# Optimization experiments

Measured on AMD Instinct MI355X. Metric: run time of the kernel, lower is better.

The kernel has to match this reference:

```python
import jax, jax.numpy as jnp
import numpy as np

B, N, DIM = 16, 1024, 768
H = 12
HD = DIM // H
SCALE = HD ** -0.5

def setup_inputs() -> dict:
    key = jax.random.key(0)
    k1, k2, k3, k4 = jax.random.split(key, 4)
    x = jax.random.normal(k1, (B, N, DIM), dtype=jnp.float32)
    # qkv: Linear(dim, 3*dim, bias=False); torch weight is [out, in]
    w_qkv = jax.random.normal(k2, (3 * DIM, DIM), dtype=jnp.float32) * (DIM ** -0.5)
    # proj: Linear(dim, dim) with bias
    w_proj = jax.random.normal(k3, (DIM, DIM), dtype=jnp.float32) * (DIM ** -0.5)
    b_proj = jax.random.normal(k4, (DIM,), dtype=jnp.float32) * 0.02
    return {"x": x, "w_qkv": w_qkv, "w_proj": w_proj, "b_proj": b_proj}

def reference(x, w_qkv, w_proj, b_proj):
    B_, N_, D_ = x.shape
    # qkv projection: [B, N, 3*D] -> [3, B, H, N, HD]
    qkv = jnp.einsum('bnd,ed->bne', x, w_qkv)
    qkv = qkv.reshape(B_, N_, 3, H, HD).transpose(2, 0, 3, 1, 4)
    q, k, v = qkv[0], qkv[1], qkv[2]
    # attention scores [B, H, N, N]
    attn = jnp.einsum('bhqd,bhkd->bhqk', q, k) * SCALE
    attn = jax.nn.softmax(attn, axis=-1)
    # weighted values -> [B, N, D]
    out = jnp.einsum('bhqk,bhkd->bhqd', attn, v)
    out = out.transpose(0, 2, 1, 3).reshape(B_, N_, D_)
    # output projection
    out = jnp.einsum('bnd,ed->bne', out, w_proj) + b_proj
    return out
```

## Files before the change

### kernel.cpp

```cpp
#include <hip/hip_runtime.h>
#include <cstdint>

#define B_SZ 16
#define SEQ 1024
#define DIM 768
#define NH 12
#define HD 64
#define M_TOTAL (B_SZ*SEQ)
#define QKV_OUT (3*DIM)
#define EXP2_SCALE 0.18033688011f

typedef _Float16 f16;
typedef __attribute__((ext_vector_type(8))) f16 f16x8;
typedef __attribute__((ext_vector_type(4))) f16 f16x4;
typedef __attribute__((ext_vector_type(2))) __fp16 pk16x2;
typedef __attribute__((ext_vector_type(4))) short s4_t;
typedef __attribute__((ext_vector_type(4))) float f32x4;
typedef unsigned int u32;
typedef const __attribute__((address_space(1))) u32* gas_t;
typedef __attribute__((address_space(3))) u32* las_t;

union U4 { pk16x2 h2[2]; f16x4 v; };
union U8 { pk16x2 h2[4]; f16x8 v; };
union HS { f16 h; short s; };

__device__ __forceinline__ void async16(const void* g, void* l) {
    __builtin_amdgcn_global_load_lds((gas_t)g, (las_t)l, 16, 0, 0);
}
__device__ __forceinline__ f32x4 mfma32h(f16x8 a, f16x8 b, f32x4 c) {
    return __builtin_amdgcn_mfma_f32_16x16x32_f16(a, b, c, 0, 0, 0);
}
__device__ __forceinline__ f16x8 ldfragh(const short* p) {
    return *(const f16x8*)p;
}

__global__ void cvt_kernel(const float* __restrict__ x, const float* __restrict__ wq,
                           const float* __restrict__ wp,
                           short* __restrict__ xb, short* __restrict__ wqb, short* __restrict__ wpb) {
    const long nx = (long)M_TOTAL * DIM / 4;
    const long nq = (long)QKV_OUT * DIM / 4;
    const long np = (long)DIM * DIM / 4;
    const long total = nx + nq + np;
    for (long i = (long)blockIdx.x * blockDim.x + threadIdx.x; i < total;
         i += (long)gridDim.x * blockDim.x) {
        const float4* src; short* dst; long off;
        if (i < nx)            { src = (const float4*)x;  dst = xb;  off = i; }
        else if (i < nx + nq)  { src = (const float4*)wq; dst = wqb; off = i - nx; }
        else                   { src = (const float4*)wp; dst = wpb; off = i - nx - nq; }
        float4 v = src[off];
        U4 u;
        u.h2[0] = __builtin_amdgcn_cvt_pkrtz(v.x, v.y);
        u.h2[1] = __builtin_amdgcn_cvt_pkrtz(v.z, v.w);
        *(f16x4*)(dst + off * 4) = u.v;
    }
}

template<int MH, int NHH>
__device__ __forceinline__ void mfma_quad(f32x4 (&acc)[4][6], const f16x8 (&af)[2][2],
                                          const f16x8 (&bf)[3][2]) {
#pragma unroll
    for (int r = 0; r < 2; ++r)
#pragma unroll
        for (int c = 0; c < 3; ++c) {
            f32x4 t = acc[MH * 2 + r][NHH * 3 + c];
            t = mfma32h(af[r][0], bf[c][0], t);
            t = mfma32h(af[r][1], bf[c][1], t);
            acc[MH * 2 + r][NHH * 3 + c] = t;
        }
}

template<int EPI, int N, int K>
__global__ __launch_bounds__(512, 2) void gemm_bt(const short* __restrict__ A,
                                                  const short* __restrict__ Bm,
                                                  short* __restrict__ Cq, short* __restrict__ Ck,
                                                  short* __restrict__ Cv,
                                                  float* __restrict__ Cout,
                                                  const float* __restrict__ bias) {
    static_assert(K % 128 == 0, "even K-tile count required");
    constexpr int NT = K / 64;
    constexpr int NIT = NT / 2;
    constexpr int SLOT = 28672;
    __shared__ short lds[2 * SLOT];

    const int tid = threadIdx.x;
    const int l = tid & 63, quad = l >> 4, l15 = l & 15, l7 = l15 & 7;
    const int w = tid >> 6, wr = w >> 1, wc = w & 1;

    const int gx = gridDim.x;
    const int nwg = gx * (int)gridDim.y;
    int fid = (int)blockIdx.y * gx + (int)blockIdx.x;
    fid = (fid & 7) * (nwg >> 3) + (fid >> 3);
    const int m0 = (fid / gx) * 256;
    const int n0 = (fid % gx) * 192;

    const int srow = tid >> 3, sc = tid & 7;
    const int scc = sc ^ (srow & 7);
    const short* Asrc = A + (size_t)(m0 + srow) * K + scc * 8;
    const short* Bsrc = Bm + (size_t)(n0 + srow) * K + scc * 8;
    const int sdst = tid * 8;

#define STAGE_A(t, u) async16(Asrc + (size_t)((u) * 64) * K + (t) * 64, \
                              &lds[((t) & 1) * SLOT + (u) * 4096 + sdst])
#define STAGE_B(t, u) async16(Bsrc + (size_t)((u) * 64) * K + (t) * 64, \
                              &lds[((t) & 1) * SLOT + 16384 + (u) * 4096 + sdst])

    const int awoff = wr * 4096 + l15 * 64;
    const int bwoff = 16384 + wc * 6144 + l15 * 64;
    const int c0 = (quad ^ l7) * 8;
    const int c1 = ((4 + quad) ^ l7) * 8;

#define RD_A(SB, MH) do {                                      \
        const int ab_ = (SB) + awoff + (MH) * 2048;            \
        af[0][0] = ldfragh(&lds[ab_ + c0]);                    \
        af[0][1] = ldfragh(&lds[ab_ + c1]);                    \
        af[1][0] = ldfragh(&lds[ab_ + 1024 + c0]);             \
        af[1][1] = ldfragh(&lds[ab_ + 1024 + c1]);             \
    } while (0)
#define RD_B(SB, NHH) do {                                     \
        const int bb_ = (SB) + bwoff + (NHH) * 3072;           \
        bf[0][0] = ldfragh(&lds[bb_ + c0]);                    \
        bf[0][1] = ldfragh(&lds[bb_ + c1]);                    \
        bf[1][0] = ldfragh(&lds[bb_ + 1024 + c0]);             \
        bf[1][1] = ldfragh(&lds[bb_ + 1024 + c1]);             \
        bf[2][0] = ldfragh(&lds[bb_ + 2048 + c0]);             \
        bf[2][1] = ldfragh(&lds[bb_ + 2048 + c1]);             \
    } while (0)

#define BAR1() __builtin_amdgcn_s_barrier()
#define BAR2() do { __builtin_amdgcn_s_barrier(); __builtin_amdgcn_sched_barrier(0); } while (0)
#define VMC3() asm volatile("s_waitcnt vmcnt(3)" ::: "memory")
#define VMC0() asm volatile("s_waitcnt vmcnt(0)" ::: "memory")
#define MQ(MH, NHH) do {                                       \
        __builtin_amdgcn_s_setprio(1);                         \
        mfma_quad<MH, NHH>(acc, af, bf);                       \
        __builtin_amdgcn_s_setprio(0);                         \
    } while (0)

    f32x4 acc[4][6];
#pragma unroll
    for (int i = 0; i < 4; ++i)
#pragma unroll
        for (int j = 0; j < 6; ++j) acc[i][j] = (f32x4){0.f, 0.f, 0.f, 0.f};
    f16x8 af[2][2], bf[3][2];

    STAGE_B(0, 0); STAGE_B(0, 1); STAGE_B(0, 2);
    STAGE_A(0, 0); STAGE_A(0, 1); STAGE_A(0, 2); STAGE_A(0, 3);
    STAGE_B(1, 0); STAGE_B(1, 1); STAGE_B(1, 2);
    VMC3();
    BAR2();

#pragma unroll 1
    for (int i = 0; i < NIT; ++i) {
        const int ta = 2 * i, tb = 2 * i + 1;
        {
            const int t1 = ta + 1, t2 = ta + 2;
            RD_A(0, 0); RD_B(0, 0);
            if (t1 < NT) { STAGE_A(t1, 0); STAGE_A(t1, 1); }
            BAR1(); MQ(0, 0); BAR2();

            RD_A(0, 1);
            if (t1 < NT) { STAGE_A(t1, 2); STAGE_A(t1, 3); }
            BAR1(); MQ(1, 0); BAR2();

            RD_B(0, 1);
            BAR1(); MQ(1, 1); BAR2();

            RD_A(0, 0);
            if (t2 < NT) { STAGE_B(t2, 0); STAGE_B(t2, 1); STAGE_B(t2, 2); }
            BAR1(); MQ(0, 1);
            if (t2 < NT) VMC3(); else VMC0();
            BAR2();
        }
        {
            const int t1 = tb + 1, t2 = tb + 2;
            RD_A(SLOT, 0); RD_B(SLOT, 0);
            if (t1 < NT) { STAGE_A(t1, 0); STAGE_A(t1, 1); }
            BAR1(); MQ(0, 0); BAR2();

            RD_A(SLOT, 1);
            if (t1 < NT) { STAGE_A(t1, 2); STAGE_A(t1, 3); }
            BAR1(); MQ(1, 0); BAR2();

            RD_B(SLOT, 1);
            BAR1(); MQ(1, 1); BAR2();

            RD_A(SLOT, 0);
            if (t2 < NT) { STAGE_B(t2, 0); STAGE_B(t2, 1); STAGE_B(t2, 2); }
            BAR1(); MQ(0, 1);
            if (t2 < NT) VMC3(); else VMC0();
            BAR2();
        }
    }
#undef STAGE_A
#undef STAGE_B
#undef RD_A
#undef RD_B

#pragma unroll
    for (int rt = 0; rt < 4; ++rt) {
        const int mrow = m0 + wr * 64 + (rt >> 1) * 32 + (rt & 1) * 16 + quad * 4;
#pragma unroll
        for (int ct = 0; ct < 6; ++ct) {
            const int col = n0 + wc * 96 + (ct / 3) * 48 + (ct % 3) * 16 + l15;
            if (EPI == 0) {
                int s = col / DIM;
                int h = (col - s * DIM) >> 6, hd = col & 63;
                int b = mrow >> 10, nn = mrow & 1023;
                if (s == 2) {
                    U4 u;
                    u.h2[0] = __builtin_amdgcn_cvt_pkrtz(acc[rt][ct][0], acc[rt][ct][1]);
                    u.h2[1] = __builtin_amdgcn_cvt_pkrtz(acc[rt][ct][2], acc[rt][ct][3]);
                    *(f16x4*)&Cv[(((size_t)b * NH + h) * HD + hd) * SEQ + nn] = u.v;
                } else {
                    short* dst = (s == 0) ? Cq : Ck;
                    const float qs = (s == 0) ? EXP2_SCALE : 1.0f;
#pragma unroll
                    for (int r = 0; r < 4; ++r) {
                        HS t; t.h = (f16)(acc[rt][ct][r] * qs);
                        dst[(((size_t)b * NH + h) * SEQ + nn + r) * HD + hd] = t.s;
                    }
                }
            } else {
                float bv = bias[col];
#pragma unroll
                for (int r = 0; r < 4; ++r)
                    Cout[(size_t)(mrow + r) * N + col] = acc[rt][ct][r] + bv;
            }
        }
    }
}

__global__ __launch_bounds__(256) void attn_kernel(const short* __restrict__ Q,
                                                   const short* __restrict__ Km,
                                                   const short* __restrict__ Vt,
                                                   short* __restrict__ O) {
    __shared__ short lds[3][8192];
    const int tid = threadIdx.x;
    const int w = tid >> 6, l = tid & 63, quad = l >> 4, l15 = l & 15;
    const int bid = blockIdx.x;
    const int xcd = bid & 7, kk = bid >> 3;
    const int head = xcd + 8 * (kk >> 2);
    const int q0 = (kk & 3) * 256 + w * 64;
    const int b = head / NH, h = head - b * NH;
    const short* Qp = Q + (size_t)head * (SEQ * HD);
    const short* Kp = Km + (size_t)head * (SEQ * HD);
    const short* Vp = Vt + (size_t)head * (SEQ * HD);

    f16x8 qf[4][2];
#pragma unroll
    for (int qt = 0; qt < 4; ++qt)
#pragma unroll
        for (int hf = 0; hf < 2; ++hf)
            qf[qt][hf] = *(const f16x8*)&Qp[(q0 + qt * 16 + l15) * HD + hf * 32 + quad * 8];

    f32x4 oacc[4][4];
#pragma unroll
    for (int qt = 0; qt < 4; ++qt)
#pragma unroll
        for (int ht = 0; ht < 4; ++ht) oacc[qt][ht] = (f32x4){0.f, 0.f, 0.f, 0.f};
    float psum[4] = {0.f, 0.f, 0.f, 0.f};

    const int kr = tid >> 3, kc = tid & 7;
    const int kcc = kc ^ ((kr & 3) ^ (((kr >> 3) & 3) << 1));
    const short* kSrc = Kp + kr * HD + kcc * 8;
    const int kDst = kr * 64 + kc * 8;
    const int vr = tid >> 2, vc = tid & 3;
    const int vcc = vc ^ ((vr >> 1) & 3);
    const short* vSrc = Vp + vr * SEQ + vcc * 8;
    const int vDst = 4096 + vr * 32 + vc * 8;

#define STAGE(bf, g) do {                                            \
        async16(kSrc + (size_t)(g) * 64 * HD, &lds[bf][kDst]);       \
        async16(kSrc + (size_t)((g) * 64 + 32) * HD,                 \
                &lds[bf][kDst + 2048]);                              \
        async16(vSrc + (g) * 64, &lds[bf][vDst]);                    \
        async16(vSrc + (g) * 64 + 32, &lds[bf][vDst + 2048]);        \
    } while (0)

    const int rA = 8 * (l15 >> 2) + (l15 & 3);
    const int sk = (l15 & 3) ^ ((l15 >> 2) << 1);
    const int offK = rA * 64 + ((quad ^ sk) * 8);
    const int offV = 4096 + l15 * 32 + ((quad ^ ((l15 >> 1) & 3)) * 8);

    STAGE(0, 0); STAGE(1, 1);

    int cur = 0, nb = 2;
    for (int g = 0; g < 16; ++g) {
        if (g <= 14) asm volatile("s_waitcnt vmcnt(4)" ::: "memory");
        else         asm volatile("s_waitcnt vmcnt(0)" ::: "memory");
        __builtin_amdgcn_s_barrier();
        if (g < 14) STAGE(nb, g + 2);

        const short* bufp = &lds[cur][0];
#pragma unroll
        for (int half = 0; half < 2; ++half) {
            const short* kb = bufp + half * 2048;
            f16x8 kA0 = ldfragh(kb + offK);
            f16x8 kA1 = ldfragh(kb + (offK ^ 32));
            f16x8 kB0 = ldfragh(kb + offK + 256);
            f16x8 kB1 = ldfragh(kb + (offK ^ 32) + 256);
            f16x8 v0 = ldfragh(kb + offV);
            f16x8 v1 = ldfragh(kb + offV + 512);
            f16x8 v2 = ldfragh(kb + offV + 1024);
            f16x8 v3 = ldfragh(kb + offV + 1536);

            __builtin_amdgcn_s_setprio(1);
#pragma unroll
            for (int qt = 0; qt < 4; ++qt) {
                f32x4 sA = (f32x4){0.f, 0.f, 0.f, 0.f};
                sA = mfma32h(kA0, qf[qt][0], sA);
                sA = mfma32h(kA1, qf[qt][1], sA);
                f32x4 sB = (f32x4){0.f, 0.f, 0.f, 0.f};
                sB = mfma32h(kB0, qf[qt][0], sB);
                sB = mfma32h(kB1, qf[qt][1], sB);
                float eA0 = __builtin_amdgcn_exp2f(sA[0]);
                float eA1 = __builtin_amdgcn_exp2f(sA[1]);
                float eA2 = __builtin_amdgcn_exp2f(sA[2]);
                float eA3 = __builtin_amdgcn_exp2f(sA[3]);
                float eB0 = __builtin_amdgcn_exp2f(sB[0]);
                float eB1 = __builtin_amdgcn_exp2f(sB[1]);
                float eB2 = __builtin_amdgcn_exp2f(sB[2]);
                float eB3 = __builtin_amdgcn_exp2f(sB[3]);
                psum[qt] += ((eA0 + eA1) + (eA2 + eA3)) + ((eB0 + eB1) + (eB2 + eB3));
                U8 u;
                u.h2[0] = __builtin_amdgcn_cvt_pkrtz(eA0, eA1);
                u.h2[1] = __builtin_amdgcn_cvt_pkrtz(eA2, eA3);
                u.h2[2] = __builtin_amdgcn_cvt_pkrtz(eB0, eB1);
                u.h2[3] = __builtin_amdgcn_cvt_pkrtz(eB2, eB3);
                oacc[qt][0] = mfma32h(v0, u.v, oacc[qt][0]);
                oacc[qt][1] = mfma32h(v1, u.v, oacc[qt][1]);
                oacc[qt][2] = mfma32h(v2, u.v, oacc[qt][2]);
                oacc[qt][3] = mfma32h(v3, u.v, oacc[qt][3]);
            }
            __builtin_amdgcn_s_setprio(0);
        }
        cur = (cur == 2) ? 0 : cur + 1;
        nb = (nb == 2) ? 0 : nb + 1;
    }
#undef STAGE

#pragma unroll
    for (int qt = 0; qt < 4; ++qt) {
        psum[qt] += __shfl_xor(psum[qt], 16);
        psum[qt] += __shfl_xor(psum[qt], 32);
    }

#pragma unroll
    for (int qt = 0; qt < 4; ++qt) {
        float rinv = 1.0f / psum[qt];
        short* orow = &O[((size_t)b * SEQ + q0 + qt * 16 + l15) * DIM + h * HD + quad * 4];
#pragma unroll
        for (int ht = 0; ht < 4; ++ht) {
            U4 u;
            u.h2[0] = __builtin_amdgcn_cvt_pkrtz(oacc[qt][ht][0] * rinv, oacc[qt][ht][1] * rinv);
            u.h2[1] = __builtin_amdgcn_cvt_pkrtz(oacc[qt][ht][2] * rinv, oacc[qt][ht][3] * rinv);
            *(f16x4*)(orow + ht * 16) = u.v;
        }
    }
}

extern "C" void kernel_launch(void* const* d_in, const int* in_sizes, int n_in,
                              void* d_out, int out_size, void* d_ws, size_t ws_size,
                              hipStream_t stream) {
    const float* x      = (const float*)d_in[0];
    const float* w_qkv  = (const float*)d_in[1];
    const float* w_proj = (const float*)d_in[2];
    const float* b_proj = (const float*)d_in[3];
    float* out = (float*)d_out;

    short* p = (short*)d_ws;
    short* Xb  = p; p += (size_t)M_TOTAL * DIM;
    short* Wqb = p; p += (size_t)QKV_OUT * DIM;
    short* Wpb = p; p += (size_t)DIM * DIM;
    short* Qb  = p; p += (size_t)B_SZ * NH * SEQ * HD;
    short* Kb  = p; p += (size_t)B_SZ * NH * SEQ * HD;
    short* Vtb = p; p += (size_t)B_SZ * NH * SEQ * HD;
    short* Ob  = p; p += (size_t)M_TOTAL * DIM;

    cvt_kernel<<<1024, 256, 0, stream>>>(x, w_qkv, w_proj, Xb, Wqb, Wpb);
    gemm_bt<0, QKV_OUT, DIM><<<dim3(QKV_OUT / 192, M_TOTAL / 256), 512, 0, stream>>>(
        Xb, Wqb, Qb, Kb, Vtb, nullptr, nullptr);
    attn_kernel<<<B_SZ * NH * (SEQ / 256), 256, 0, stream>>>(Qb, Kb, Vtb, Ob);
    gemm_bt<1, DIM, DIM><<<dim3(DIM / 192, M_TOTAL / 256), 512, 0, stream>>>(
        Ob, Wpb, nullptr, nullptr, nullptr, out, b_proj);
}
```

Baseline: 275.3 us.

## Restructure GEMM k-loop to load all fragments then issue all MFMAs per tile

Replaces the four-phase interleaved schedule, which alternated LDS fragment reads, partial MFMA quads and staggered async stages, with a simpler per-tile body. Each tile now waits on vmcnt, loads all A and B fragments from LDS at once, runs the full 4x6 MFMA block, and then issues the async loads for tile t+2. The epilogue row and column mapping changes to match the flat fragment indexing. This removes barriers and phase bookkeeping but needs more fragment registers and cuts the overlap of LDS reads with MFMA work and of global loads with compute.

```diff
diff --git a/kernel.cpp b/kernel.cpp
--- a/kernel.cpp
+++ b/kernel.cpp
@@ -55,20 +55,6 @@
     }
 }
 
-template<int MH, int NHH>
-__device__ __forceinline__ void mfma_quad(f32x4 (&acc)[4][6], const f16x8 (&af)[2][2],
-                                          const f16x8 (&bf)[3][2]) {
-#pragma unroll
-    for (int r = 0; r < 2; ++r)
-#pragma unroll
-        for (int c = 0; c < 3; ++c) {
-            f32x4 t = acc[MH * 2 + r][NHH * 3 + c];
-            t = mfma32h(af[r][0], bf[c][0], t);
-            t = mfma32h(af[r][1], bf[c][1], t);
-            acc[MH * 2 + r][NHH * 3 + c] = t;
-        }
-}
-
 template<int EPI, int N, int K>
 __global__ __launch_bounds__(512, 2) void gemm_bt(const short* __restrict__ A,
                                                   const short* __restrict__ Bm,
@@ -109,31 +95,50 @@
     const int c0 = (quad ^ l7) * 8;
     const int c1 = ((4 + quad) ^ l7) * 8;
 
-#define RD_A(SB, MH) do {                                      \
-        const int ab_ = (SB) + awoff + (MH) * 2048;            \
-        af[0][0] = ldfragh(&lds[ab_ + c0]);                    \
-        af[0][1] = ldfragh(&lds[ab_ + c1]);                    \
-        af[1][0] = ldfragh(&lds[ab_ + 1024 + c0]);             \
-        af[1][1] = ldfragh(&lds[ab_ + 1024 + c1]);             \
+#define RD_ALL(SB) do {                                                                        \
+        const int ab_ = (SB) + awoff;                                                          \
+        af[0][0] = ldfragh(&lds[ab_ + c0]);        af[0][1] = ldfragh(&lds[ab_ + c1]);         \
+        af[1][0] = ldfragh(&lds[ab_ + 1024 + c0]); af[1][1] = ldfragh(&lds[ab_ + 1024 + c1]);  \
+        af[2][0] = ldfragh(&lds[ab_ + 2048 + c0]); af[2][1] = ldfragh(&lds[ab_ + 2048 + c1]);  \
+        af[3][0] = ldfragh(&lds[ab_ + 3072 + c0]); af[3][1] = ldfragh(&lds[ab_ + 3072 + c1]);  \
+        const int bb_ = (SB) + bwoff;                                                          \
+        bf[0][0] = ldfragh(&lds[bb_ + c0]);        bf[0][1] = ldfragh(&lds[bb_ + c1]);         \
+        bf[1][0] = ldfragh(&lds[bb_ + 1024 + c0]); bf[1][1] = ldfragh(&lds[bb_ + 1024 + c1]);  \
+        bf[2][0] = ldfragh(&lds[bb_ + 2048 + c0]); bf[2][1] = ldfragh(&lds[bb_ + 2048 + c1]);  \
+        bf[3][0] = ldfragh(&lds[bb_ + 3072 + c0]); bf[3][1] = ldfragh(&lds[bb_ + 3072 + c1]);  \
+        bf[4][0] = ldfragh(&lds[bb_ + 4096 + c0]); bf[4][1] = ldfragh(&lds[bb_ + 4096 + c1]);  \
+        bf[5][0] = ldfragh(&lds[bb_ + 5120 + c0]); bf[5][1] = ldfragh(&lds[bb_ + 5120 + c1]);  \
     } while (0)
-#define RD_B(SB, NHH) do {                                     \
-        const int bb_ = (SB) + bwoff + (NHH) * 3072;           \
-        bf[0][0] = ldfragh(&lds[bb_ + c0]);                    \
-        bf[0][1] = ldfragh(&lds[bb_ + c1]);                    \
-        bf[1][0] = ldfragh(&lds[bb_ + 1024 + c0]);             \
-        bf[1][1] = ldfragh(&lds[bb_ + 1024 + c1]);             \
-        bf[2][0] = ldfragh(&lds[bb_ + 2048 + c0]);             \
-        bf[2][1] = ldfragh(&lds[bb_ + 2048 + c1]);             \
+
+#define BAR2() do { __builtin_amdgcn_s_barrier(); __builtin_amdgcn_sched_barrier(0); } while (0)
+#define VMC7() asm volatile("s_waitcnt vmcnt(7)" ::: "memory")
+#define VMC0() asm volatile("s_waitcnt vmcnt(0)" ::: "memory")
+
+#define MFMA_ALL() do {                                        \
+        _Pragma("unroll")                                      \
+        for (int rt = 0; rt < 4; ++rt)                         \
+            _Pragma("unroll")                                  \
+            for (int ct = 0; ct < 6; ++ct) {                   \
+                f32x4 tacc = acc[rt][ct];                      \
+                tacc = mfma32h(af[rt][0], bf[ct][0], tacc);    \
+                tacc = mfma32h(af[rt][1], bf[ct][1], tacc);    \
+                acc[rt][ct] = tacc;                            \
+            }                                                  \
     } while (0)
 
-#define BAR1() __builtin_amdgcn_s_barrier()
-#define BAR2() do { __builtin_amdgcn_s_barrier(); __builtin_amdgcn_sched_barrier(0); } while (0)
-#define VMC3() asm volatile("s_waitcnt vmcnt(3)" ::: "memory")
-#define VMC0() asm volatile("s_waitcnt vmcnt(0)" ::: "memory")
-#define MQ(MH, NHH) do {                                       \
-        __builtin_amdgcn_s_setprio(1);                         \
-        mfma_quad<MH, NHH>(acc, af, bf);                       \
-        __builtin_amdgcn_s_setprio(0);                         \
+#define TILE_BODY(t, SB) do {                                                  \
+        if ((t) < NT - 1) VMC7(); else VMC0();                                 \
+        BAR2();                                                                \
+        RD_ALL(SB);                                                            \
+        __builtin_amdgcn_s_setprio(1);                                         \
+        MFMA_ALL();                                                            \
+        __builtin_amdgcn_s_setprio(0);                                         \
+        BAR2();                                                                \
+        if ((t) + 2 < NT) {                                                    \
+            STAGE_A((t) + 2, 0); STAGE_A((t) + 2, 1);                          \
+            STAGE_A((t) + 2, 2); STAGE_A((t) + 2, 3);                          \
+            STAGE_B((t) + 2, 0); STAGE_B((t) + 2, 1); STAGE_B((t) + 2, 2);     \
+        }                                                                      \
     } while (0)
 
     f32x4 acc[4][6];
@@ -141,67 +146,30 @@
     for (int i = 0; i < 4; ++i)
 #pragma unroll
         for (int j = 0; j < 6; ++j) acc[i][j] = (f32x4){0.f, 0.f, 0.f, 0.f};
-    f16x8 af[2][2], bf[3][2];
-
+    f16x8 af[4][2], bf[6][2];
+
+    STAGE_A(0, 0); STAGE_A(0, 1); STAGE_A(0, 2); STAGE_A(0, 3);
     STAGE_B(0, 0); STAGE_B(0, 1); STAGE_B(0, 2);
-    STAGE_A(0, 0); STAGE_A(0, 1); STAGE_A(0, 2); STAGE_A(0, 3);
+    STAGE_A(1, 0); STAGE_A(1, 1); STAGE_A(1, 2); STAGE_A(1, 3);
     STAGE_B(1, 0); STAGE_B(1, 1); STAGE_B(1, 2);
-    VMC3();
-    BAR2();
 
 #pragma unroll 1
     for (int i = 0; i < NIT; ++i) {
-        const int ta = 2 * i, tb = 2 * i + 1;
-        {
-            const int t1 = ta + 1, t2 = ta + 2;
-            RD_A(0, 0); RD_B(0, 0);
-            if (t1 < NT) { STAGE_A(t1, 0); STAGE_A(t1, 1); }
-            BAR1(); MQ(0, 0); BAR2();
-
-            RD_A(0, 1);
-            if (t1 < NT) { STAGE_A(t1, 2); STAGE_A(t1, 3); }
-            BAR1(); MQ(1, 0); BAR2();
-
-            RD_B(0, 1);
-            BAR1(); MQ(1, 1); BAR2();
-
-            RD_A(0, 0);
-            if (t2 < NT) { STAGE_B(t2, 0); STAGE_B(t2, 1); STAGE_B(t2, 2); }
-            BAR1(); MQ(0, 1);
-            if (t2 < NT) VMC3(); else VMC0();
-            BAR2();
-        }
-        {
-            const int t1 = tb + 1, t2 = tb + 2;
-            RD_A(SLOT, 0); RD_B(SLOT, 0);
-            if (t1 < NT) { STAGE_A(t1, 0); STAGE_A(t1, 1); }
-            BAR1(); MQ(0, 0); BAR2();
-
-            RD_A(SLOT, 1);
-            if (t1 < NT) { STAGE_A(t1, 2); STAGE_A(t1, 3); }
-            BAR1(); MQ(1, 0); BAR2();
-
-            RD_B(SLOT, 1);
-            BAR1(); MQ(1, 1); BAR2();
-
-            RD_A(SLOT, 0);
-            if (t2 < NT) { STAGE_B(t2, 0); STAGE_B(t2, 1); STAGE_B(t2, 2); }
-            BAR1(); MQ(0, 1);
-            if (t2 < NT) VMC3(); else VMC0();
-            BAR2();
-        }
+        TILE_BODY(2 * i, 0);
+        TILE_BODY(2 * i + 1, SLOT);
     }
 #undef STAGE_A
 #undef STAGE_B
-#undef RD_A
-#undef RD_B
+#undef RD_ALL
+#undef MFMA_ALL
+#undef TILE_BODY
 
 #pragma unroll
     for (int rt = 0; rt < 4; ++rt) {
-        const int mrow = m0 + wr * 64 + (rt >> 1) * 32 + (rt & 1) * 16 + quad * 4;
+        const int mrow = m0 + wr * 64 + rt * 16 + quad * 4;
 #pragma unroll
         for (int ct = 0; ct < 6; ++ct) {
-            const int col = n0 + wc * 96 + (ct / 3) * 48 + (ct % 3) * 16 + l15;
+            const int col = n0 + wc * 96 + ct * 16 + l15;
             if (EPI == 0) {
                 int s = col / DIM;
                 int h = (col - s * DIM) >> 6, hd = col & 63;
@@ -274,7 +242,7 @@
         async16(kSrc + (size_t)((g) * 64 + 32) * HD,                 \
                 &lds[bf][kDst + 2048]);                              \
         async16(vSrc + (g) * 64, &lds[bf][vDst]);                    \
-        async16(vSrc + (g) * 64 + 32, &lds[bf][vDst + 2048]);        \
+        async16(vSrc + (g) * 64 + 32, &lds[bf][vDst + 2048]);       \
     } while (0)
 
     const int rA = 8 * (l15 >> 2) + (l15 & 3);
```

After: 264.9 us. -3.8%, faster.
